# Performance work log

Hardware: AMD Instinct MI355X
Metric: run time of the kernel (lower is better)

## Reference

```python
import jax, jax.numpy as jnp
import numpy as np

B, K, D = 262144, 100, 384
MOMENTUM = 0.95
EPS = 1e-8  # matches F.cosine_similarity eps clamp


def setup_inputs() -> dict:
    key = jax.random.key(0)
    k1, k2 = jax.random.split(key)
    embeddings = jax.random.normal(k1, (B, D), dtype=jnp.float32)
    centroids = jax.random.normal(k2, (K, D), dtype=jnp.float32)
    counts = jnp.zeros((K,), dtype=jnp.float32)
    return {"embeddings": embeddings, "centroids": centroids, "counts": counts}


def reference(embeddings, centroids, counts):
    # Batched version of compute_novelty: cosine similarity of each embedding
    # against every active cluster centroid (all K treated as active).
    e = embeddings / jnp.maximum(jnp.linalg.norm(embeddings, axis=-1, keepdims=True), EPS)
    c = centroids / jnp.maximum(jnp.linalg.norm(centroids, axis=-1, keepdims=True), EPS)
    sims = jnp.einsum('bd,kd->bk', e, c)            # [B, K] cosine similarities
    max_sim = jnp.max(sims, axis=-1)                # [B]
    closest = jnp.argmax(sims, axis=-1)             # [B] int
    novelty = 1.0 - max_sim * max_sim               # squared-distance novelty (FIX 4)

    # Batched EMA centroid update (update_cluster fused over the batch):
    # each cluster moves toward the mean of the embeddings assigned to it.
    num_k = centroids.shape[0]
    seg_sum = jax.ops.segment_sum(embeddings, closest, num_segments=num_k)   # [K, D]
    seg_cnt = jax.ops.segment_sum(jnp.ones((embeddings.shape[0],), embeddings.dtype),
                                  closest, num_segments=num_k)               # [K]
    seg_mean = seg_sum / jnp.maximum(seg_cnt, 1.0)[:, None]
    hit = (seg_cnt > 0)[:, None]
    new_centroids = jnp.where(hit, MOMENTUM * centroids + (1.0 - MOMENTUM) * seg_mean,
                              centroids)
    new_counts = counts + seg_cnt
    return novelty, closest, new_centroids, new_counts
```

## Files before the change

kernel.cpp:

```cpp
#include <hip/hip_runtime.h>
#include <math.h>

#define B_N 262144
#define K_N 100
#define D_N 384
#define EPS 1e-8f
#define MOM 0.95f
#define FLAG_THR 5e-4f
#define NBLK 256
#define ROWS_PB (B_N / NBLK)
#define KSTR 101
#define PART_N (K_N * D_N)

typedef __attribute__((ext_vector_type(8))) short short8;
typedef __attribute__((ext_vector_type(4))) float f32x4;

#define OFF_CPK   0
#define OFF_NC64  86016
#define OFF_CNT   86816
#define OFF_FLAGN 87264
#define OFF_FLAGS 87328
#define OFF_PARTS 1135904

#define GLOAD_LDS(g, l) __builtin_amdgcn_global_load_lds( \
    (const __attribute__((address_space(1))) unsigned int*)(g), \
    (__attribute__((address_space(3))) unsigned int*)(l), 16, 0, 0)

__device__ __forceinline__ size_t cpk_idx(int col, int d) {
    int kk = d >> 5, r = d & 31, lg = r >> 3, j = r & 7;
    int nt = col >> 4, l15 = col & 15;
    return (size_t)((kk * 7 + nt) * 512) + lg * 128 + l15 * 8 + j;
}

__device__ __forceinline__ unsigned short bf16_rne(float x) {
    unsigned u = __float_as_uint(x);
    unsigned r = (u + 0x7fff + ((u >> 16) & 1)) >> 16;
    return (unsigned short)r;
}

__global__ void k_norm_c(const float* __restrict__ c, unsigned short* __restrict__ cpk,
                         double* __restrict__ nc64, int* __restrict__ cnt,
                         int* __restrict__ flagn) {
    int col = blockIdx.x;
    int t = threadIdx.x;
    if (col == 112) {
        if (t < K_N) cnt[t] = 0;
        if (t == 0) *flagn = 0;
        return;
    }
    if (col >= K_N) {
        for (int d = t; d < D_N; d += 128) cpk[cpk_idx(col, d)] = 0;
        return;
    }
    const float* row = c + (size_t)col * D_N;
    double ss = 0.0;
    for (int d = t; d < D_N; d += 128) { double v = row[d]; ss += v * v; }
    __shared__ double red[2];
    for (int o = 32; o > 0; o >>= 1) ss += __shfl_down(ss, o);
    if ((t & 63) == 0) red[t >> 6] = ss;
    __syncthreads();
    double nc = fmax(sqrt(red[0] + red[1]), (double)EPS);
    if (t == 0) nc64[col] = nc;
    float inv = (float)(1.0 / nc);
    for (int d = t; d < D_N; d += 128)
        cpk[cpk_idx(col, d)] = bf16_rne(row[d] * inv);
}

__device__ __forceinline__ void splitA(float4 x0, float4 x1,
                                       short8& ah, short8& al, float& ss) {
    float xs[8] = {x0.x, x0.y, x0.z, x0.w, x1.x, x1.y, x1.z, x1.w};
#pragma unroll
    for (int j = 0; j < 8; j++) {
        float x = xs[j];
        unsigned xb = __float_as_uint(x);
        unsigned hb = xb & 0xffff0000u;
        float lf = x - __uint_as_float(hb);
        ah[j] = (short)(hb >> 16);
        al[j] = (short)bf16_rne(lf);
        ss = fmaf(x, x, ss);
    }
}

__global__ __launch_bounds__(512) void k_main(
    const float* __restrict__ e, const unsigned short* __restrict__ cpk,
    float* __restrict__ out_nov, float* __restrict__ out_cls,
    unsigned* __restrict__ flags, int* __restrict__ flagn) {
    __shared__ unsigned short sB[84 * 512];
    __shared__ float sA[2][128][64];
    const int t = threadIdx.x;
    const int lane = t & 63;
    const int wid = t >> 6;
    const int l15 = lane & 15;
    const int lg = lane >> 4;
    const int rowbase = blockIdx.x * 128;

    for (int c = wid; c < 84; c += 8)
        GLOAD_LDS((const char*)cpk + c * 1024 + lane * 16,
                  (char*)sB + c * 1024);

#pragma unroll
    for (int i = 0; i < 4; i++) {
        int c = i * 8 + wid;
        const float* src = e + (size_t)(rowbase + c * 4 + (lane >> 4)) * D_N
                             + (lane & 15) * 4;
        GLOAD_LDS(src, &sA[0][c * 4][0]);
    }

    f32x4 acc[7];
#pragma unroll
    for (int nt = 0; nt < 7; nt++) acc[nt] = f32x4{0.f, 0.f, 0.f, 0.f};
    float ss0 = 0.f;

    __syncthreads();

#pragma unroll
    for (int g = 0; g < 6; g++) {
        if (g < 5) {
            const int nb = (g + 1) & 1;
#pragma unroll
            for (int i = 0; i < 4; i++) {
                int c = i * 8 + wid;
                const float* src = e + (size_t)(rowbase + c * 4 + (lane >> 4)) * D_N
                                     + (g + 1) * 64 + (lane & 15) * 4;
                GLOAD_LDS(src, &sA[nb][c * 4][0]);
            }
        }
#pragma unroll
        for (int j = 0; j < 2; j++) {
            const int kk = g * 2 + j;
            const float* ap = &sA[g & 1][wid * 16 + l15][j * 32 + lg * 8];
            float4 x0 = *(const float4*)ap;
            float4 x1 = *(const float4*)(ap + 4);
            short8 ah0, al0;
            splitA(x0, x1, ah0, al0, ss0);
#pragma unroll
            for (int nt = 0; nt < 7; nt++) {
                short8 bh = *(const short8*)(sB + (kk * 7 + nt) * 512 + lane * 8);
                acc[nt] = __builtin_amdgcn_mfma_f32_16x16x32_bf16(ah0, bh, acc[nt], 0, 0, 0);
                acc[nt] = __builtin_amdgcn_mfma_f32_16x16x32_bf16(al0, bh, acc[nt], 0, 0, 0);
            }
        }
        __syncthreads();
    }

    ss0 += __shfl_xor(ss0, 16); ss0 += __shfl_xor(ss0, 32);
    const int rl = lg * 4 + (l15 & 3);
    float ssr0 = __shfl(ss0, rl);

    float b0 = -3e38f, b1 = -3e38f, b2 = -3e38f, b3 = -3e38f;
    float s0 = -3e38f, s1 = -3e38f, s2 = -3e38f, s3 = -3e38f;
    int i0 = 0, i1 = 0, i2 = 0, i3 = 0, j0 = 0, j1 = 0, j2 = 0, j3 = 0;
#pragma unroll
    for (int nt = 0; nt < 7; nt++) {
        int cl = nt * 16 + l15;
        bool valid = cl < K_N;
        float v;
        v = valid ? acc[nt][0] : -3e38f;
        if (v > b0) { s0 = b0; j0 = i0; b0 = v; i0 = cl; } else if (v > s0) { s0 = v; j0 = cl; }
        v = valid ? acc[nt][1] : -3e38f;
        if (v > b1) { s1 = b1; j1 = i1; b1 = v; i1 = cl; } else if (v > s1) { s1 = v; j1 = cl; }
        v = valid ? acc[nt][2] : -3e38f;
        if (v > b2) { s2 = b2; j2 = i2; b2 = v; i2 = cl; } else if (v > s2) { s2 = v; j2 = cl; }
        v = valid ? acc[nt][3] : -3e38f;
        if (v > b3) { s3 = b3; j3 = i3; b3 = v; i3 = cl; } else if (v > s3) { s3 = v; j3 = cl; }
    }
#pragma unroll
    for (int w = 1; w <= 8; w <<= 1) {
#define MRG(B, S, I, J)                                                        \
        {                                                                      \
            float ob = __shfl_xor(B, w), os = __shfl_xor(S, w);                \
            int obi = __shfl_xor(I, w), osi = __shfl_xor(J, w);                \
            if (ob > B) {                                                      \
                float ns; int nsi;                                             \
                if (B > os) { ns = B; nsi = I; } else { ns = os; nsi = osi; }  \
                B = ob; I = obi; S = ns; J = nsi;                              \
            } else if (ob > S) { S = ob; J = obi; }                            \
        }
        MRG(b0, s0, i0, j0) MRG(b1, s1, i1, j1) MRG(b2, s2, i2, j2) MRG(b3, s3, i3, j3)
#undef MRG
    }
    if (l15 < 4) {
        float bb = (l15 & 2) ? ((l15 & 1) ? b3 : b2) : ((l15 & 1) ? b1 : b0);
        float sv = (l15 & 2) ? ((l15 & 1) ? s3 : s2) : ((l15 & 1) ? s1 : s0);
        int bi   = (l15 & 2) ? ((l15 & 1) ? i3 : i2) : ((l15 & 1) ? i1 : i0);
        int si   = (l15 & 2) ? ((l15 & 1) ? j3 : j2) : ((l15 & 1) ? j1 : j0);
        int grow = rowbase + wid * 16 + rl;
        float nrm = fmaxf(sqrtf(ssr0), EPS);
        float msim = bb / nrm;
        out_nov[grow] = 1.f - msim * msim;
        out_cls[grow] = (float)bi;
        if (bb - sv < FLAG_THR * nrm) {
            int pos = atomicAdd(flagn, 1);
            flags[pos] = ((unsigned)grow << 14) | ((unsigned)bi << 7) | (unsigned)si;
        }
    }
}

__global__ void k_refine(const float* __restrict__ e, const float* __restrict__ c_raw,
                         const double* __restrict__ nc64, const int* __restrict__ flagn,
                         const unsigned* __restrict__ flags,
                         float* __restrict__ out_nov, float* __restrict__ out_cls) {
    int n = *flagn;
    int gw = (blockIdx.x * 256 + threadIdx.x) >> 6;
    int lane = threadIdx.x & 63;
    int nw = (gridDim.x * 256) >> 6;
    for (int i = gw; i < n; i += nw) {
        unsigned f = flags[i];
        int row = f >> 14, bi = (f >> 7) & 127, si = f & 127;
        const float* er = e + (size_t)row * D_N;
        const float* ca = c_raw + (size_t)bi * D_N;
        const float* cb = c_raw + (size_t)si * D_N;
        double d1 = 0, d2 = 0, ee = 0;
#pragma unroll
        for (int j = 0; j < 6; j++) {
            int d = lane * 6 + j;
            double ev = er[d];
            d1 += ev * (double)ca[d];
            d2 += ev * (double)cb[d];
            ee += ev * ev;
        }
#pragma unroll
        for (int w = 1; w <= 32; w <<= 1) {
            d1 += __shfl_xor(d1, w); d2 += __shfl_xor(d2, w); ee += __shfl_xor(ee, w);
        }
        if (lane == 0) {
            double v1 = d1 / nc64[bi], v2 = d2 / nc64[si];
            int k; double v;
            if (v2 > v1 || (v2 == v1 && si < bi)) { k = si; v = v2; } else { k = bi; v = v1; }
            double nrm = fmax(sqrt(ee), (double)EPS);
            double ms = v / nrm;
            out_nov[row] = (float)(1.0 - ms * ms);
            out_cls[row] = (float)k;
        }
    }
}

__global__ __launch_bounds__(768) void k_accum(
    const float* __restrict__ e, const float* __restrict__ cls,
    int* __restrict__ parts, int* __restrict__ cnt) {
    __shared__ int sums[D_N * KSTR];
    __shared__ int scls[ROWS_PB];
    __shared__ int h[K_N];
    const int t = threadIdx.x;
    const int rg = t / D_N;
    const int d = t - rg * D_N;
    const size_t rbase = (size_t)blockIdx.x * ROWS_PB;

    for (int i = t; i < D_N * KSTR; i += 768) sums[i] = 0;
    if (t < K_N) h[t] = 0;
    __syncthreads();
    for (int i = t; i < ROWS_PB; i += 768) {
        int k = (int)cls[rbase + i];
        scls[i] = k;
        atomicAdd(&h[k], 1);
    }
    __syncthreads();
    if (t < K_N && h[t] > 0) atomicAdd(&cnt[t], h[t]);

    const float* eb = e + rbase * D_N;
    for (int g = 0; g < ROWS_PB; g += 16) {
        const int r0 = g + rg,      r1 = g + rg + 2,  r2 = g + rg + 4,  r3 = g + rg + 6;
        const int r4 = g + rg + 8,  r5 = g + rg + 10, r6 = g + rg + 12, r7 = g + rg + 14;
        float v0 = eb[(size_t)r0 * D_N + d]; float v1 = eb[(size_t)r1 * D_N + d];
        float v2 = eb[(size_t)r2 * D_N + d]; float v3 = eb[(size_t)r3 * D_N + d];
        float v4 = eb[(size_t)r4 * D_N + d]; float v5 = eb[(size_t)r5 * D_N + d];
        float v6 = eb[(size_t)r6 * D_N + d]; float v7 = eb[(size_t)r7 * D_N + d];
        atomicAdd(&sums[d * KSTR + scls[r0]], __float2int_rn(v0 * 65536.f));
        atomicAdd(&sums[d * KSTR + scls[r1]], __float2int_rn(v1 * 65536.f));
        atomicAdd(&sums[d * KSTR + scls[r2]], __float2int_rn(v2 * 65536.f));
        atomicAdd(&sums[d * KSTR + scls[r3]], __float2int_rn(v3 * 65536.f));
        atomicAdd(&sums[d * KSTR + scls[r4]], __float2int_rn(v4 * 65536.f));
        atomicAdd(&sums[d * KSTR + scls[r5]], __float2int_rn(v5 * 65536.f));
        atomicAdd(&sums[d * KSTR + scls[r6]], __float2int_rn(v6 * 65536.f));
        atomicAdd(&sums[d * KSTR + scls[r7]], __float2int_rn(v7 * 65536.f));
    }
    __syncthreads();

    int* pb = parts + (size_t)blockIdx.x * PART_N;
    for (int i = t; i < PART_N; i += 768) {
        int k = i / K_N == 0 ? 0 : 0, dd = 0;
        (void)k; (void)dd;
        int kq = i / D_N, dr = i - kq * D_N;
        pb[i] = sums[dr * KSTR + kq];
    }
}

__global__ void k_reduce(const float* __restrict__ c_raw, const int* __restrict__ parts,
                         const int* __restrict__ cnt, const float* __restrict__ counts_in,
                         float* __restrict__ out_cent, float* __restrict__ out_cnts) {
    int idx = blockIdx.x * 256 + threadIdx.x;
    if (blockIdx.x == 0 && threadIdx.x < K_N)
        out_cnts[threadIdx.x] = counts_in[threadIdx.x] + (float)cnt[threadIdx.x];
    if (idx >= PART_N) return;
    long long s = 0;
#pragma unroll 8
    for (int b = 0; b < NBLK; b++) s += (long long)parts[(size_t)b * PART_N + idx];
    int k = idx / D_N;
    int n = cnt[k];
    float c0 = c_raw[idx];
    float mean = (float)((double)s / 65536.0 / (double)(n > 1 ? n : 1));
    out_cent[idx] = (n > 0) ? (MOM * c0 + (1.0f - MOM) * mean) : c0;
}

extern "C" void kernel_launch(void* const* d_in, const int* in_sizes, int n_in,
                              void* d_out, int out_size, void* d_ws, size_t ws_size,
                              hipStream_t stream) {
    const float* emb    = (const float*)d_in[0];
    const float* cen    = (const float*)d_in[1];
    const float* counts = (const float*)d_in[2];
    float* out = (float*)d_out;
    char* ws = (char*)d_ws;

    unsigned short* cpk   = (unsigned short*)(ws + OFF_CPK);
    double*         nc64  = (double*)(ws + OFF_NC64);
    int*            cnt   = (int*)(ws + OFF_CNT);
    int*            flagn = (int*)(ws + OFF_FLAGN);
    unsigned*       flags = (unsigned*)(ws + OFF_FLAGS);
    int*            parts = (int*)(ws + OFF_PARTS);

    float* out_nov  = out;
    float* out_cls  = out + B_N;
    float* out_cent = out + 2 * B_N;
    float* out_cnts = out + 2 * B_N + K_N * D_N;

    k_norm_c<<<113, 128, 0, stream>>>(cen, cpk, nc64, cnt, flagn);
    k_main<<<B_N / 128, 512, 0, stream>>>(emb, cpk, out_nov, out_cls, flags, flagn);
    k_refine<<<256, 256, 0, stream>>>(emb, cen, nc64, flagn, flags, out_nov, out_cls);
    k_accum<<<NBLK, 768, 0, stream>>>(emb, out_cls, parts, cnt);
    k_reduce<<<(PART_N + 255) / 256, 256, 0, stream>>>(cen, parts, cnt, counts,
                                                       out_cent, out_cnts);
}
```

Baseline: 273.8 us.

## Split K dimension across wave halves in k_main with smaller row tiles

k_main now processes 64 rows per block instead of 128, loading the whole row tile into padded LDS at once rather than double-buffering 64-column chunks. The two halves of the eight waves each cover half of the reduction dimension and merge their accumulators through LDS. Only the first 5 of 7 centroid tiles are staged in LDS; the last two are read directly from global memory. The goal is more parallelism and less per-step synchronisation, at the cost of a 157 KB LDS footprint (one block per CU), an extra merge pass, and global loads inside the MFMA loop.

```diff
diff --git a/kernel.cpp b/kernel.cpp
--- a/kernel.cpp
+++ b/kernel.cpp
@@ -81,66 +81,95 @@
     }
 }
 
+#define SA_STRIDE 1552
 __global__ __launch_bounds__(512) void k_main(
     const float* __restrict__ e, const unsigned short* __restrict__ cpk,
     float* __restrict__ out_nov, float* __restrict__ out_cls,
     unsigned* __restrict__ flags, int* __restrict__ flagn) {
-    __shared__ unsigned short sB[84 * 512];
-    __shared__ float sA[2][128][64];
+    __shared__ char smem[160768];
+    float* sA = (float*)smem;
+    unsigned short* sB = (unsigned short*)(smem + 99328);
+    float* mrg = (float*)smem;
+
     const int t = threadIdx.x;
     const int lane = t & 63;
     const int wid = t >> 6;
     const int l15 = lane & 15;
     const int lg = lane >> 4;
-    const int rowbase = blockIdx.x * 128;
-
-    for (int c = wid; c < 84; c += 8)
-        GLOAD_LDS((const char*)cpk + c * 1024 + lane * 16,
+    const int rowbase = blockIdx.x * 64;
+
+    for (int c = wid; c < 60; c += 8) {
+        int kk = c / 5, nt = c - kk * 5;
+        GLOAD_LDS((const char*)cpk + (size_t)(kk * 7 + nt) * 1024 + lane * 16,
                   (char*)sB + c * 1024);
-
-#pragma unroll
-    for (int i = 0; i < 4; i++) {
-        int c = i * 8 + wid;
-        const float* src = e + (size_t)(rowbase + c * 4 + (lane >> 4)) * D_N
-                             + (lane & 15) * 4;
-        GLOAD_LDS(src, &sA[0][c * 4][0]);
-    }
+    }
+
+#pragma unroll
+    for (int q = 0; q < 4; q++) {
+        const char* gb = (const char*)e + ((size_t)(rowbase + wid * 8 + 2 * q)) * 1536;
+#pragma unroll
+        for (int i = 0; i < 3; i++) {
+            int byt = i * 1024 + lane * 16;
+            float4 v = *(const float4*)(gb + byt);
+            int r = (byt >= 1536) ? 1 : 0;
+            int off = byt - r * 1536;
+            *(float4*)((char*)sA + (size_t)(wid * 8 + 2 * q + r) * SA_STRIDE + off) = v;
+        }
+    }
+    __syncthreads();
 
     f32x4 acc[7];
 #pragma unroll
     for (int nt = 0; nt < 7; nt++) acc[nt] = f32x4{0.f, 0.f, 0.f, 0.f};
     float ss0 = 0.f;
 
-    __syncthreads();
-
-#pragma unroll
-    for (int g = 0; g < 6; g++) {
-        if (g < 5) {
-            const int nb = (g + 1) & 1;
-#pragma unroll
-            for (int i = 0; i < 4; i++) {
-                int c = i * 8 + wid;
-                const float* src = e + (size_t)(rowbase + c * 4 + (lane >> 4)) * D_N
-                                     + (g + 1) * 64 + (lane & 15) * 4;
-                GLOAD_LDS(src, &sA[nb][c * 4][0]);
-            }
-        }
-#pragma unroll
-        for (int j = 0; j < 2; j++) {
-            const int kk = g * 2 + j;
-            const float* ap = &sA[g & 1][wid * 16 + l15][j * 32 + lg * 8];
-            float4 x0 = *(const float4*)ap;
-            float4 x1 = *(const float4*)(ap + 4);
-            short8 ah0, al0;
-            splitA(x0, x1, ah0, al0, ss0);
-#pragma unroll
-            for (int nt = 0; nt < 7; nt++) {
-                short8 bh = *(const short8*)(sB + (kk * 7 + nt) * 512 + lane * 8);
-                acc[nt] = __builtin_amdgcn_mfma_f32_16x16x32_bf16(ah0, bh, acc[nt], 0, 0, 0);
-                acc[nt] = __builtin_amdgcn_mfma_f32_16x16x32_bf16(al0, bh, acc[nt], 0, 0, 0);
-            }
-        }
-        __syncthreads();
+    const int p = wid & 3;
+    const int kk0 = (wid < 4) ? 0 : 6;
+    const int arow = p * 16 + l15;
+
+#pragma unroll
+    for (int u = 0; u < 6; u++) {
+        const int kk = kk0 + u;
+        const char* ap = (const char*)sA + (size_t)arow * SA_STRIDE + kk * 128 + lg * 32;
+        float4 x0 = *(const float4*)ap;
+        float4 x1 = *(const float4*)(ap + 16);
+        short8 ah0, al0;
+        splitA(x0, x1, ah0, al0, ss0);
+#pragma unroll
+        for (int nt = 0; nt < 5; nt++) {
+            short8 bh = *(const short8*)(sB + (kk * 5 + nt) * 512 + lane * 8);
+            acc[nt] = __builtin_amdgcn_mfma_f32_16x16x32_bf16(ah0, bh, acc[nt], 0, 0, 0);
+            acc[nt] = __builtin_amdgcn_mfma_f32_16x16x32_bf16(al0, bh, acc[nt], 0, 0, 0);
+        }
+#pragma unroll
+        for (int nt = 5; nt < 7; nt++) {
+            short8 bh = *(const short8*)(cpk + (kk * 7 + nt) * 512 + lane * 8);
+            acc[nt] = __builtin_amdgcn_mfma_f32_16x16x32_bf16(ah0, bh, acc[nt], 0, 0, 0);
+            acc[nt] = __builtin_amdgcn_mfma_f32_16x16x32_bf16(al0, bh, acc[nt], 0, 0, 0);
+        }
+    }
+    __syncthreads();
+
+    if (wid >= 4) {
+        float* mb = mrg + ((size_t)(wid - 4) * 64 + lane) * 33;
+#pragma unroll
+        for (int nt = 0; nt < 7; nt++) {
+            mb[nt * 4 + 0] = acc[nt][0]; mb[nt * 4 + 1] = acc[nt][1];
+            mb[nt * 4 + 2] = acc[nt][2]; mb[nt * 4 + 3] = acc[nt][3];
+        }
+        mb[28] = ss0;
+    }
+    __syncthreads();
+    if (wid >= 4) return;
+
+    {
+        const float* mb = mrg + ((size_t)wid * 64 + lane) * 33;
+#pragma unroll
+        for (int nt = 0; nt < 7; nt++) {
+            acc[nt][0] += mb[nt * 4 + 0]; acc[nt][1] += mb[nt * 4 + 1];
+            acc[nt][2] += mb[nt * 4 + 2]; acc[nt][3] += mb[nt * 4 + 3];
+        }
+        ss0 += mb[28];
     }
 
     ss0 += __shfl_xor(ss0, 16); ss0 += __shfl_xor(ss0, 32);
@@ -278,8 +307,6 @@
 
     int* pb = parts + (size_t)blockIdx.x * PART_N;
     for (int i = t; i < PART_N; i += 768) {
-        int k = i / K_N == 0 ? 0 : 0, dd = 0;
-        (void)k; (void)dd;
         int kq = i / D_N, dr = i - kq * D_N;
         pb[i] = sums[dr * KSTR + kq];
     }
@@ -324,7 +351,7 @@
     float* out_cnts = out + 2 * B_N + K_N * D_N;
 
     k_norm_c<<<113, 128, 0, stream>>>(cen, cpk, nc64, cnt, flagn);
-    k_main<<<B_N / 128, 512, 0, stream>>>(emb, cpk, out_nov, out_cls, flags, flagn);
+    k_main<<<B_N / 64, 512, 0, stream>>>(emb, cpk, out_nov, out_cls, flags, flagn);
     k_refine<<<256, 256, 0, stream>>>(emb, cen, nc64, flagn, flags, out_nov, out_cls);
     k_accum<<<NBLK, 768, 0, stream>>>(emb, out_cls, parts, cnt);
     k_reduce<<<(PART_N + 255) / 256, 256, 0, stream>>>(cen, parts, cnt, counts,
```

Measured after the change: 291.3 us. +6.4%, slower.
